# Optimization experiments

Measured on AMD Instinct MI355X. Metric: run time of the kernel, lower is better.

The kernel has to match this reference:

```python
import jax, jax.numpy as jnp
import numpy as np

WIDTH = 4096
NUM_HEADS = 8
BLOCK_W = WIDTH // NUM_HEADS


def _block_diag_linear(x, w, b):
    # x: [n, width] -> [n, h, bw]; w: [h, bw, bw]; b: [h, bw]
    n = x.shape[0]
    xh = x.reshape(n, NUM_HEADS, BLOCK_W)
    y = jnp.einsum('nhi,hij->nhj', xh, w) + b
    return y.reshape(n, WIDTH)


def setup_inputs() -> dict:
    key = jax.random.key(0)
    ks = jax.random.split(key, 7)
    n = 8192
    x = jax.random.normal(ks[0], (n, WIDTH), dtype=jnp.float32)
    s = jnp.sort(jax.random.randint(ks[1], (n,), 0, 8, dtype=jnp.int32))
    # a_param init: uniform on ring radii [0.9, 0.999], softplus-inverse transform
    eps = 1e-8
    u = jax.random.uniform(ks[2], (WIDTH,), minval=0.9**2 + eps, maxval=0.999**2 + eps)
    t = 0.5 * jnp.log(u)
    a_param = jnp.log(jnp.exp(-t) - 1.0).astype(jnp.float32)
    std = 1.0 / np.sqrt(BLOCK_W)
    ig_w = std * jax.random.normal(ks[3], (NUM_HEADS, BLOCK_W, BLOCK_W), dtype=jnp.float32)
    ig_b = jnp.zeros((NUM_HEADS, BLOCK_W), dtype=jnp.float32)
    ag_w = std * jax.random.normal(ks[4], (NUM_HEADS, BLOCK_W, BLOCK_W), dtype=jnp.float32)
    ag_b = jnp.zeros((NUM_HEADS, BLOCK_W), dtype=jnp.float32)
    return {'x': x, 's': s, 'a_param': a_param, 'ig_w': ig_w, 'ig_b': ig_b,
            'ag_w': ag_w, 'ag_b': ag_b}


def reference(x, s, a_param, ig_w, ig_b, ag_w, ag_b):
    n, k = x.shape
    # reset mask: True at position 0 and wherever segment id changes
    reset = jnp.concatenate([jnp.ones((1,), dtype=bool), s[1:] != s[:-1]])
    gate_x = jax.nn.sigmoid(_block_diag_linear(x, ig_w, ig_b))
    gate_a = jax.nn.sigmoid(_block_diag_linear(x, ag_w, ag_b))
    log_a = -8.0 * gate_a * jax.nn.softplus(a_param)  # [n, k]
    a = jnp.exp(log_a)
    a_square = jnp.exp(2.0 * log_a)
    multiplier = jnp.sqrt(1.0 - a_square)
    multiplier = jnp.where(reset[:, None], 1.0, multiplier)
    normalized_x = x * gate_x * multiplier
    # linear recurrence h[t] = a[t] * h[t-1] + normalized_x[t] via parallel scan
    def combine(e1, e2):
        a1, b1 = e1
        a2, b2 = e2
        return (a1 * a2, a2 * b1 + b2)
    _, out = jax.lax.associative_scan(combine, (a, normalized_x), axis=0)
    return out
```

## Files before the change

kernel.cpp:

```cpp
#include <hip/hip_runtime.h>
#include <hip/hip_bf16.h>
#include <stdint.h>

#define WIDTH 4096
#define NROWS 8192
#define NHEADS 8
#define BW 512
#define CS 128
#define NCHUNK (NROWS/CS)

typedef short bf16x8 __attribute__((ext_vector_type(8)));
typedef float f32x4 __attribute__((ext_vector_type(4)));

__device__ __forceinline__ uint32_t rne_bf16(float f) {
  uint32_t u = __float_as_uint(f);
  return (u + 0x7fffu + ((u >> 16) & 1u)) >> 16;
}
__device__ __forceinline__ uint32_t pack2(float lo, float hi) {
  return rne_bf16(lo) | (rne_bf16(hi) << 16);
}
__device__ __forceinline__ float bf16_to_f32(uint32_t bits) {
  return __uint_as_float(bits << 16);
}

__device__ __forceinline__ void gload_lds16(const void* g, void* l) {
  __builtin_amdgcn_global_load_lds(
      (const __attribute__((address_space(1))) void*)g,
      (__attribute__((address_space(3))) void*)l, 16, 0, 0);
}

__global__ void prep_xbf16(const float* __restrict__ x, uint16_t* __restrict__ xb) {
  size_t i = ((size_t)blockIdx.x * 256 + threadIdx.x) * 8;
  float4 f0 = *reinterpret_cast<const float4*>(x + i);
  float4 f1 = *reinterpret_cast<const float4*>(x + i + 4);
  uint4 v;
  v.x = pack2(f0.x, f0.y); v.y = pack2(f0.z, f0.w);
  v.z = pack2(f1.x, f1.y); v.w = pack2(f1.z, f1.w);
  *reinterpret_cast<uint4*>(xb + i) = v;
}

__global__ void prep_weights(const float* __restrict__ ig_w,
                             const float* __restrict__ ag_w,
                             uint16_t* __restrict__ wt) {
  __shared__ float tile[32][33];
  int j0 = blockIdx.x * 32;
  int i0 = blockIdx.y * 32;
  int m  = blockIdx.z;
  const float* src = ((m >> 3) ? ag_w : ig_w) + (size_t)(m & 7) * BW * BW;
  int tx = threadIdx.x & 31, ty = threadIdx.x >> 5;
  #pragma unroll
  for (int k = 0; k < 4; k++) {
    int i = i0 + ty + 8 * k;
    tile[ty + 8 * k][tx] = src[(size_t)i * BW + (j0 + tx)];
  }
  __syncthreads();
  #pragma unroll
  for (int k = 0; k < 4; k++) {
    int j = j0 + ty + 8 * k;
    wt[((size_t)m * BW + j) * BW + (i0 + tx)] = (uint16_t)rne_bf16(tile[tx][ty + 8 * k]);
  }
}

__global__ void prep_misc(const float* __restrict__ a_param, float* __restrict__ cvec) {
  int i = blockIdx.x * 256 + threadIdx.x;
  if (i < WIDTH) {
    float x = a_param[i];
    float sp = (x > 15.f) ? x : log1pf(expf(x));
    cvec[i] = 8.f * sp;
  }
}

#define BM 128
#define BN 64
#define BK 64

__global__ __launch_bounds__(256, 4)
void gates_gemm(const uint16_t* __restrict__ xb,
                const int* __restrict__ s,
                const uint16_t* __restrict__ wt,
                const float* __restrict__ ig_b,
                const float* __restrict__ ag_b,
                const float* __restrict__ cvec,
                uint32_t* __restrict__ lanx,
                float* __restrict__ cA,
                float* __restrict__ cB) {
  __shared__ __align__(16) unsigned char dsm[32768];
  __shared__ unsigned char resetm[BM];

  const int b = blockIdx.x;
  const int orig = (b & 7) * 512 + (b >> 3);
  const int h  = orig >> 9;
  const int rem = orig & 511;
  const int mt = rem >> 3;
  const int nt = rem & 7;
  const int m0 = mt * BM;
  const int j0 = nt * BN;

  const int tid = threadIdx.x;
  const int lane = tid & 63;
  const int w = tid >> 6;
  const int wr = w >> 1;
  const int wc = w & 1;
  const int lrow = lane & 15;
  const int lkg  = lane >> 4;

  if (tid < BM) {
    int n = m0 + tid;
    resetm[tid] = (n == 0) || (s[n] != s[n - 1]);
  }

  const char* xb_src[4];
  #pragma unroll
  for (int i = 0; i < 4; i++) {
    int o = i * 4096 + tid * 16;
    int row = o >> 7;
    int c = (o & 127) ^ ((row & 7) << 4);
    xb_src[i] = (const char*)xb + (size_t)(m0 + row) * (WIDTH * 2) + h * (BW * 2) + c;
  }
  const char* w_src[4];
  #pragma unroll
  for (int i = 0; i < 4; i++) {
    int o = i * 4096 + tid * 16;
    int g = o >> 13;
    int jl = (o >> 7) & 63;
    int c = (o & 127) ^ ((jl & 7) << 4);
    w_src[i] = (const char*)wt + ((size_t)((g * 8 + h) * BW + (j0 + jl))) * (BW * 2) + c;
  }

  f32x4 acc[2][4][2];
  #pragma unroll
  for (int g = 0; g < 2; g++)
    #pragma unroll
    for (int mf = 0; mf < 4; mf++)
      #pragma unroll
      for (int nf = 0; nf < 2; nf++)
        acc[g][mf][nf] = (f32x4){0.f, 0.f, 0.f, 0.f};

  for (int kt = 0; kt < 8; kt++) {
    const int p = (nt + 1 + kt) & 7;
    __syncthreads();
    #pragma unroll
    for (int i = 0; i < 4; i++)
      gload_lds16(xb_src[i] + p * 128, dsm + i * 4096 + tid * 16);
    #pragma unroll
    for (int i = 0; i < 4; i++)
      gload_lds16(w_src[i] + p * 128, dsm + 16384 + i * 4096 + tid * 16);
    __syncthreads();
    #pragma unroll
    for (int ks = 0; ks < 2; ks++) {
      bf16x8 af[4];
      #pragma unroll
      for (int mf = 0; mf < 4; mf++) {
        int row = wr * 64 + 16 * mf + lrow;
        uint32_t addr = (uint32_t)((row << 7) + ks * 64 + lkg * 16);
        addr ^= (uint32_t)((row & 7) << 4);
        af[mf] = *reinterpret_cast<const bf16x8*>(dsm + addr);
      }
      #pragma unroll
      for (int g = 0; g < 2; g++) {
        #pragma unroll
        for (int nf = 0; nf < 2; nf++) {
          int j = wc * 32 + 16 * nf + lrow;
          uint32_t addr = (uint32_t)(16384 + (g << 13) + (j << 7) + ks * 64 + lkg * 16);
          addr ^= (uint32_t)((j & 7) << 4);
          bf16x8 bfr = *reinterpret_cast<const bf16x8*>(dsm + addr);
          #pragma unroll
          for (int mf = 0; mf < 4; mf++) {
            acc[g][mf][nf] = __builtin_amdgcn_mfma_f32_16x16x32_bf16(
                af[mf], bfr, acc[g][mf][nf], 0, 0, 0);
          }
        }
      }
    }
  }
  __syncthreads();

  float* smf = (float*)(dsm + 16384);

  #pragma unroll
  for (int nf = 0; nf < 2; nf++) {
    int jl = wc * 32 + 16 * nf + lrow;
    int jj = h * BW + j0 + jl;
    const int cc2 = jl * 2;
    float igb = ig_b[jj], agb = ag_b[jj], cv = cvec[jj];
    float segA[4], segB[4];
    #pragma unroll
    for (int mf = 0; mf < 4; mf++) {
      float A = 1.f, B = 0.f;
      int rbase = wr * 64 + 16 * mf + 4 * lkg;
      #pragma unroll
      for (int r = 0; r < 4; r++) {
        int row = rbase + r;
        int n = m0 + row;
        size_t o = (size_t)n * WIDTH + jj;
        float yig = acc[0][mf][nf][r] + igb;
        float yag = acc[1][mf][nf][r] + agb;
        float gx = __builtin_amdgcn_rcpf(1.f + __expf(-yig));
        float ga = __builtin_amdgcn_rcpf(1.f + __expf(-yag));
        float la = -ga * cv;
        uint32_t la_bits = rne_bf16(la);
        float la_r = bf16_to_f32(la_bits);
        float a = __expf(la_r);
        float mult = resetm[row] ? 1.f
                     : __builtin_amdgcn_sqrtf(fmaxf(1.f - a * a, 0.f));
        uint32_t xaddr = (uint32_t)((row << 7) + cc2) ^ (uint32_t)((row & 7) << 4);
        float xv = bf16_to_f32(*reinterpret_cast<const uint16_t*>(dsm + xaddr));
        float nx = xv * gx * mult;
        uint32_t nx_bits = rne_bf16(nx);
        float nx_r = bf16_to_f32(nx_bits);
        lanx[o] = la_bits | (nx_bits << 16);
        A *= a;
        B = fmaf(a, B, nx_r);
      }
      segA[mf] = A; segB[mf] = B;
    }
    #pragma unroll
    for (int mf = 0; mf < 4; mf++) {
      float A = segA[mf], B = segB[mf];
      #pragma unroll
      for (int d = 16; d <= 32; d <<= 1) {
        float pA = __shfl_xor(A, d, 64);
        float pB = __shfl_xor(B, d, 64);
        bool up = (lane & d) != 0;
        B = up ? fmaf(A, pB, B) : fmaf(pA, B, pB);
        A *= pA;
      }
      segA[mf] = A; segB[mf] = B;
    }
    float colA = segA[0], colB = segB[0];
    #pragma unroll
    for (int mf = 1; mf < 4; mf++) {
      colB = fmaf(segA[mf], colB, segB[mf]);
      colA *= segA[mf];
    }
    if (lkg == 0) {
      int clocal = wc * 32 + 16 * nf + lrow;
      smf[wr * 64 + clocal] = colA;
      smf[128 + wr * 64 + clocal] = colB;
    }
  }
  __syncthreads();
  if (tid < BN) {
    float A0 = smf[tid],       B0 = smf[128 + tid];
    float A1 = smf[64 + tid],  B1 = smf[192 + tid];
    float Af = A0 * A1;
    float Bf = fmaf(A1, B0, B1);
    int jj = h * BW + j0 + tid;
    cA[mt * WIDTH + jj] = Af;
    cB[mt * WIDTH + jj] = Bf;
  }
}

__global__ void scan_prefix(const float* __restrict__ cA, const float* __restrict__ cB,
                            float* __restrict__ prefix) {
  int c = blockIdx.x * 256 + threadIdx.x;
  float hcur = 0.f;
  for (int i0 = 0; i0 < NCHUNK; i0 += 8) {
    float av[8], bv[8];
    #pragma unroll
    for (int e = 0; e < 8; e++) { av[e] = cA[(i0 + e) * WIDTH + c]; bv[e] = cB[(i0 + e) * WIDTH + c]; }
    #pragma unroll
    for (int e = 0; e < 8; e++) { prefix[(i0 + e) * WIDTH + c] = hcur; hcur = av[e] * hcur + bv[e]; }
  }
}

__global__ void scan_apply(const uint32_t* __restrict__ lanx,
                           const float* __restrict__ prefix,
                           float* __restrict__ out) {
  int chunk = blockIdx.x;
  int c0 = (blockIdx.y * 256 + threadIdx.x) * 4;
  size_t base = (size_t)chunk * CS * WIDTH + c0;
  float h[4];
  #pragma unroll
  for (int q = 0; q < 4; q++) h[q] = prefix[chunk * WIDTH + c0 + q];
  for (int rb = 0; rb < CS; rb += 4) {
    uint4 v[4];
    #pragma unroll
    for (int e = 0; e < 4; e++)
      v[e] = *reinterpret_cast<const uint4*>(lanx + base + (size_t)(rb + e) * WIDTH);
    #pragma unroll
    for (int e = 0; e < 4; e++) {
      float4 ov;
      h[0] = fmaf(__expf(bf16_to_f32(v[e].x & 0xffffu)), h[0], bf16_to_f32(v[e].x >> 16)); ov.x = h[0];
      h[1] = fmaf(__expf(bf16_to_f32(v[e].y & 0xffffu)), h[1], bf16_to_f32(v[e].y >> 16)); ov.y = h[1];
      h[2] = fmaf(__expf(bf16_to_f32(v[e].z & 0xffffu)), h[2], bf16_to_f32(v[e].z >> 16)); ov.z = h[2];
      h[3] = fmaf(__expf(bf16_to_f32(v[e].w & 0xffffu)), h[3], bf16_to_f32(v[e].w >> 16)); ov.w = h[3];
      *reinterpret_cast<float4*>(out + base + (size_t)(rb + e) * WIDTH) = ov;
    }
  }
}

extern "C" void kernel_launch(void* const* d_in, const int* in_sizes, int n_in,
                              void* d_out, int out_size, void* d_ws, size_t ws_size,
                              hipStream_t stream) {
  const float* x       = (const float*)d_in[0];
  const int*   s       = (const int*)d_in[1];
  const float* a_param = (const float*)d_in[2];
  const float* ig_w    = (const float*)d_in[3];
  const float* ig_b    = (const float*)d_in[4];
  const float* ag_w    = (const float*)d_in[5];
  const float* ag_b    = (const float*)d_in[6];
  float* out = (float*)d_out;
  char* ws = (char*)d_ws;

  uint32_t* lanx   = (uint32_t*)ws;
  uint16_t* wt     = (uint16_t*)(ws + 134217728);
  uint16_t* xb     = (uint16_t*)(ws + 142606336);
  float*    cvec   = (float*)(ws + 209715200);
  float*    cA     = (float*)(ws + 209731584);
  float*    cB     = (float*)(ws + 210780160);
  float*    prefix = (float*)(ws + 211828736);

  prep_xbf16<<<dim3(16384), 256, 0, stream>>>(x, xb);
  prep_weights<<<dim3(16, 16, 16), 256, 0, stream>>>(ig_w, ag_w, wt);
  prep_misc<<<dim3(16), 256, 0, stream>>>(a_param, cvec);
  gates_gemm<<<dim3(4096), 256, 0, stream>>>(xb, s, wt, ig_b, ag_b, cvec,
                                             lanx, cA, cB);
  scan_prefix<<<dim3(16), 256, 0, stream>>>(cA, cB, prefix);
  scan_apply<<<dim3(NCHUNK, 4), 256, 0, stream>>>(lanx, prefix, out);
}
```

Measured before the change: 224.7 us.

## Fuse x bf16 conversion into GEMM by loading fp32 x tiles into LDS

Removes the separate prep kernel that converted x to bf16. The GEMM now streams fp32 x tiles straight into a larger LDS buffer and converts them to bf16 in registers with v_cvt_pk_bf16_f32 before the MFMA. This drops a full read and write pass over x, but each GEMM block now reads twice as many x bytes. The larger LDS footprint also lowers the occupancy target from 4 to 3 blocks. The epilogue loop is reordered to handle both column fragments per row, and the epilogue now uses fp32 x values rather than bf16-rounded ones.

```diff
diff --git a/kernel.cpp b/kernel.cpp
--- a/kernel.cpp
+++ b/kernel.cpp
@@ -22,21 +22,16 @@
 __device__ __forceinline__ float bf16_to_f32(uint32_t bits) {
   return __uint_as_float(bits << 16);
 }
+__device__ __forceinline__ uint32_t cvtpk(float a, float b) {
+  uint32_t r;
+  asm("v_cvt_pk_bf16_f32 %0, %1, %2" : "=v"(r) : "v"(a), "v"(b));
+  return r;
+}
 
 __device__ __forceinline__ void gload_lds16(const void* g, void* l) {
   __builtin_amdgcn_global_load_lds(
       (const __attribute__((address_space(1))) void*)g,
       (__attribute__((address_space(3))) void*)l, 16, 0, 0);
-}
-
-__global__ void prep_xbf16(const float* __restrict__ x, uint16_t* __restrict__ xb) {
-  size_t i = ((size_t)blockIdx.x * 256 + threadIdx.x) * 8;
-  float4 f0 = *reinterpret_cast<const float4*>(x + i);
-  float4 f1 = *reinterpret_cast<const float4*>(x + i + 4);
-  uint4 v;
-  v.x = pack2(f0.x, f0.y); v.y = pack2(f0.z, f0.w);
-  v.z = pack2(f1.x, f1.y); v.w = pack2(f1.z, f1.w);
-  *reinterpret_cast<uint4*>(xb + i) = v;
 }
 
 __global__ void prep_weights(const float* __restrict__ ig_w,
@@ -74,8 +69,8 @@
 #define BN 64
 #define BK 64
 
-__global__ __launch_bounds__(256, 4)
-void gates_gemm(const uint16_t* __restrict__ xb,
+__global__ __launch_bounds__(256, 3)
+void gates_gemm(const float* __restrict__ x,
                 const int* __restrict__ s,
                 const uint16_t* __restrict__ wt,
                 const float* __restrict__ ig_b,
@@ -84,7 +79,7 @@
                 uint32_t* __restrict__ lanx,
                 float* __restrict__ cA,
                 float* __restrict__ cB) {
-  __shared__ __align__(16) unsigned char dsm[32768];
+  __shared__ __align__(16) unsigned char dsm[49152];
   __shared__ unsigned char resetm[BM];
 
   const int b = blockIdx.x;
@@ -109,13 +104,13 @@
     resetm[tid] = (n == 0) || (s[n] != s[n - 1]);
   }
 
-  const char* xb_src[4];
-  #pragma unroll
-  for (int i = 0; i < 4; i++) {
+  const char* x_src[8];
+  #pragma unroll
+  for (int i = 0; i < 8; i++) {
     int o = i * 4096 + tid * 16;
-    int row = o >> 7;
-    int c = (o & 127) ^ ((row & 7) << 4);
-    xb_src[i] = (const char*)xb + (size_t)(m0 + row) * (WIDTH * 2) + h * (BW * 2) + c;
+    int row = o >> 8;
+    int c = (o & 255) ^ ((row & 7) << 5);
+    x_src[i] = (const char*)x + ((size_t)(m0 + row) * WIDTH + h * BW) * 4 + c;
   }
   const char* w_src[4];
   #pragma unroll
@@ -140,11 +135,11 @@
     const int p = (nt + 1 + kt) & 7;
     __syncthreads();
     #pragma unroll
+    for (int i = 0; i < 8; i++)
+      gload_lds16(x_src[i] + p * 256, dsm + i * 4096 + tid * 16);
+    #pragma unroll
     for (int i = 0; i < 4; i++)
-      gload_lds16(xb_src[i] + p * 128, dsm + i * 4096 + tid * 16);
-    #pragma unroll
-    for (int i = 0; i < 4; i++)
-      gload_lds16(w_src[i] + p * 128, dsm + 16384 + i * 4096 + tid * 16);
+      gload_lds16(w_src[i] + p * 128, dsm + 32768 + i * 4096 + tid * 16);
     __syncthreads();
     #pragma unroll
     for (int ks = 0; ks < 2; ks++) {
@@ -152,16 +147,23 @@
       #pragma unroll
       for (int mf = 0; mf < 4; mf++) {
         int row = wr * 64 + 16 * mf + lrow;
-        uint32_t addr = (uint32_t)((row << 7) + ks * 64 + lkg * 16);
-        addr ^= (uint32_t)((row & 7) << 4);
-        af[mf] = *reinterpret_cast<const bf16x8*>(dsm + addr);
+        uint32_t addr = (uint32_t)((row << 8) + ks * 128 + lkg * 32);
+        addr ^= (uint32_t)((row & 7) << 5);
+        f32x4 lo = *reinterpret_cast<const f32x4*>(dsm + addr);
+        f32x4 hi = *reinterpret_cast<const f32x4*>(dsm + addr + 16);
+        union { uint32_t u[4]; bf16x8 v; } cvu;
+        cvu.u[0] = cvtpk(lo.x, lo.y);
+        cvu.u[1] = cvtpk(lo.z, lo.w);
+        cvu.u[2] = cvtpk(hi.x, hi.y);
+        cvu.u[3] = cvtpk(hi.z, hi.w);
+        af[mf] = cvu.v;
       }
       #pragma unroll
       for (int g = 0; g < 2; g++) {
         #pragma unroll
         for (int nf = 0; nf < 2; nf++) {
           int j = wc * 32 + 16 * nf + lrow;
-          uint32_t addr = (uint32_t)(16384 + (g << 13) + (j << 7) + ks * 64 + lkg * 16);
+          uint32_t addr = (uint32_t)(32768 + (g << 13) + (j << 7) + ks * 64 + lkg * 16);
           addr ^= (uint32_t)((j & 7) << 4);
           bf16x8 bfr = *reinterpret_cast<const bf16x8*>(dsm + addr);
           #pragma unroll
@@ -175,48 +177,58 @@
   }
   __syncthreads();
 
-  float* smf = (float*)(dsm + 16384);
-
+  float* smf = (float*)(dsm + 32768);
+
+  const int jl0 = wc * 32 + lrow;
+  float igb[2], agb[2], cv2[2];
   #pragma unroll
   for (int nf = 0; nf < 2; nf++) {
-    int jl = wc * 32 + 16 * nf + lrow;
-    int jj = h * BW + j0 + jl;
-    const int cc2 = jl * 2;
-    float igb = ig_b[jj], agb = ag_b[jj], cv = cvec[jj];
-    float segA[4], segB[4];
-    #pragma unroll
-    for (int mf = 0; mf < 4; mf++) {
-      float A = 1.f, B = 0.f;
-      int rbase = wr * 64 + 16 * mf + 4 * lkg;
-      #pragma unroll
-      for (int r = 0; r < 4; r++) {
-        int row = rbase + r;
-        int n = m0 + row;
-        size_t o = (size_t)n * WIDTH + jj;
-        float yig = acc[0][mf][nf][r] + igb;
-        float yag = acc[1][mf][nf][r] + agb;
+    int jj = h * BW + j0 + jl0 + 16 * nf;
+    igb[nf] = ig_b[jj]; agb[nf] = ag_b[jj]; cv2[nf] = cvec[jj];
+  }
+
+  float segA[2][4], segB[2][4];
+  #pragma unroll
+  for (int mf = 0; mf < 4; mf++) {
+    float A[2] = {1.f, 1.f}, B[2] = {0.f, 0.f};
+    int rbase = wr * 64 + 16 * mf + 4 * lkg;
+    #pragma unroll
+    for (int r = 0; r < 4; r++) {
+      int row = rbase + r;
+      int n = m0 + row;
+      bool rs = resetm[row] != 0;
+      #pragma unroll
+      for (int nf = 0; nf < 2; nf++) {
+        int jl = jl0 + 16 * nf;
+        size_t o = (size_t)n * WIDTH + h * BW + j0 + jl;
+        float yig = acc[0][mf][nf][r] + igb[nf];
+        float yag = acc[1][mf][nf][r] + agb[nf];
         float gx = __builtin_amdgcn_rcpf(1.f + __expf(-yig));
         float ga = __builtin_amdgcn_rcpf(1.f + __expf(-yag));
-        float la = -ga * cv;
+        float la = -ga * cv2[nf];
         uint32_t la_bits = rne_bf16(la);
         float la_r = bf16_to_f32(la_bits);
         float a = __expf(la_r);
-        float mult = resetm[row] ? 1.f
+        float mult = rs ? 1.f
                      : __builtin_amdgcn_sqrtf(fmaxf(1.f - a * a, 0.f));
-        uint32_t xaddr = (uint32_t)((row << 7) + cc2) ^ (uint32_t)((row & 7) << 4);
-        float xv = bf16_to_f32(*reinterpret_cast<const uint16_t*>(dsm + xaddr));
+        uint32_t xaddr = (uint32_t)((row << 8) + jl * 4) ^ (uint32_t)((row & 7) << 5);
+        float xv = *reinterpret_cast<const float*>(dsm + xaddr);
         float nx = xv * gx * mult;
         uint32_t nx_bits = rne_bf16(nx);
         float nx_r = bf16_to_f32(nx_bits);
         lanx[o] = la_bits | (nx_bits << 16);
-        A *= a;
-        B = fmaf(a, B, nx_r);
+        A[nf] *= a;
+        B[nf] = fmaf(a, B[nf], nx_r);
       }
-      segA[mf] = A; segB[mf] = B;
-    }
+    }
+    segA[0][mf] = A[0]; segB[0][mf] = B[0];
+    segA[1][mf] = A[1]; segB[1][mf] = B[1];
+  }
+  #pragma unroll
+  for (int nf = 0; nf < 2; nf++) {
     #pragma unroll
     for (int mf = 0; mf < 4; mf++) {
-      float A = segA[mf], B = segB[mf];
+      float A = segA[nf][mf], B = segB[nf][mf];
       #pragma unroll
       for (int d = 16; d <= 32; d <<= 1) {
         float pA = __shfl_xor(A, d, 64);
@@ -225,13 +237,13 @@
         B = up ? fmaf(A, pB, B) : fmaf(pA, B, pB);
         A *= pA;
       }
-      segA[mf] = A; segB[mf] = B;
-    }
-    float colA = segA[0], colB = segB[0];
+      segA[nf][mf] = A; segB[nf][mf] = B;
+    }
+    float colA = segA[nf][0], colB = segB[nf][0];
     #pragma unroll
     for (int mf = 1; mf < 4; mf++) {
-      colB = fmaf(segA[mf], colB, segB[mf]);
-      colA *= segA[mf];
+      colB = fmaf(segA[nf][mf], colB, segB[nf][mf]);
+      colA *= segA[nf][mf];
     }
     if (lkg == 0) {
       int clocal = wc * 32 + 16 * nf + lrow;
@@ -305,16 +317,14 @@
 
   uint32_t* lanx   = (uint32_t*)ws;
   uint16_t* wt     = (uint16_t*)(ws + 134217728);
-  uint16_t* xb     = (uint16_t*)(ws + 142606336);
-  float*    cvec   = (float*)(ws + 209715200);
-  float*    cA     = (float*)(ws + 209731584);
-  float*    cB     = (float*)(ws + 210780160);
-  float*    prefix = (float*)(ws + 211828736);
-
-  prep_xbf16<<<dim3(16384), 256, 0, stream>>>(x, xb);
+  float*    cvec   = (float*)(ws + 142606336);
+  float*    cA     = (float*)(ws + 142622720);
+  float*    cB     = (float*)(ws + 143671296);
+  float*    prefix = (float*)(ws + 144719872);
+
   prep_weights<<<dim3(16, 16, 16), 256, 0, stream>>>(ig_w, ag_w, wt);
   prep_misc<<<dim3(16), 256, 0, stream>>>(a_param, cvec);
-  gates_gemm<<<dim3(4096), 256, 0, stream>>>(xb, s, wt, ig_b, ag_b, cvec,
+  gates_gemm<<<dim3(4096), 256, 0, stream>>>(x, s, wt, ig_b, ag_b, cvec,
                                              lanx, cA, cB);
   scan_prefix<<<dim3(16), 256, 0, stream>>>(cA, cB, prefix);
   scan_apply<<<dim3(NCHUNK, 4), 256, 0, stream>>>(lanx, prefix, out);
```

After: 199.6 us. -11.2%, faster.

## Fuse chunk scan into gates GEMM with decoupled look-back across chunks

Applied to the files above, without the earlier changes.

The separate scan_prefix and scan_apply kernels are replaced by a single-pass decoupled look-back scan inside the gates GEMM. Blocks take an atomic ticket so chunks are processed in order, publish their chunk aggregates and inclusive prefixes through flags, and write the final output directly from registers. This removes the 128MB packed intermediate write and re-read plus two kernel launches. In exchange it adds register pressure (launch bounds lowered to 3), inter-block spin-waiting, and a small zeroing kernel.

```diff
diff --git a/kernel.cpp b/kernel.cpp
--- a/kernel.cpp
+++ b/kernel.cpp
@@ -7,7 +7,9 @@
 #define NHEADS 8
 #define BW 512
 #define CS 128
-#define NCHUNK (NROWS/CS)
+#define NCHUNK 64
+#define NGROUP 64
+#define NSLOT 65
 
 typedef short bf16x8 __attribute__((ext_vector_type(8)));
 typedef float f32x4 __attribute__((ext_vector_type(4)));
@@ -70,33 +72,51 @@
   }
 }
 
+__global__ void zero_sync(uint32_t* __restrict__ flags, float* __restrict__ Hbuf,
+                          uint32_t* __restrict__ ticket) {
+  int i = blockIdx.x * 256 + threadIdx.x;
+  if (i < NGROUP * NSLOT) flags[i] = ((i % NSLOT) == 0) ? 2u : 0u;
+  if (i < NGROUP * 64) {
+    int g = i >> 6, t = i & 63;
+    Hbuf[(size_t)(g * NSLOT) * 64 + t] = 0.f;
+  }
+  if (i == 0) *ticket = 0u;
+}
+
 #define BM 128
 #define BN 64
 #define BK 64
 
-__global__ __launch_bounds__(256, 4)
+__global__ __launch_bounds__(256, 3)
 void gates_gemm(const uint16_t* __restrict__ xb,
                 const int* __restrict__ s,
                 const uint16_t* __restrict__ wt,
                 const float* __restrict__ ig_b,
                 const float* __restrict__ ag_b,
                 const float* __restrict__ cvec,
-                uint32_t* __restrict__ lanx,
-                float* __restrict__ cA,
-                float* __restrict__ cB) {
+                float* __restrict__ out,
+                float* __restrict__ aggA,
+                float* __restrict__ aggB,
+                float* __restrict__ Hbuf,
+                uint32_t* __restrict__ flags,
+                uint32_t* __restrict__ ticket) {
   __shared__ __align__(16) unsigned char dsm[32768];
   __shared__ unsigned char resetm[BM];
-
-  const int b = blockIdx.x;
-  const int orig = (b & 7) * 512 + (b >> 3);
-  const int h  = orig >> 9;
-  const int rem = orig & 511;
-  const int mt = rem >> 3;
-  const int nt = rem & 7;
-  const int m0 = mt * BM;
+  __shared__ int tkshare;
+  __shared__ int kshare;
+
+  const int tid = threadIdx.x;
+  if (tid == 0) tkshare = (int)atomicAdd(ticket, 1u);
+  __syncthreads();
+  const int tk = tkshare;
+  const int c  = tk >> 6;
+  const int g  = tk & 63;
+  const int h  = g >> 3;
+  const int nt = g & 7;
+  const int m0 = c * BM;
   const int j0 = nt * BN;
-
-  const int tid = threadIdx.x;
+  const int sc = c + 1;
+
   const int lane = tid & 63;
   const int w = tid >> 6;
   const int wr = w >> 1;
@@ -114,27 +134,27 @@
   for (int i = 0; i < 4; i++) {
     int o = i * 4096 + tid * 16;
     int row = o >> 7;
-    int c = (o & 127) ^ ((row & 7) << 4);
-    xb_src[i] = (const char*)xb + (size_t)(m0 + row) * (WIDTH * 2) + h * (BW * 2) + c;
+    int cc = (o & 127) ^ ((row & 7) << 4);
+    xb_src[i] = (const char*)xb + (size_t)(m0 + row) * (WIDTH * 2) + h * (BW * 2) + cc;
   }
   const char* w_src[4];
   #pragma unroll
   for (int i = 0; i < 4; i++) {
     int o = i * 4096 + tid * 16;
-    int g = o >> 13;
+    int gg = o >> 13;
     int jl = (o >> 7) & 63;
-    int c = (o & 127) ^ ((jl & 7) << 4);
-    w_src[i] = (const char*)wt + ((size_t)((g * 8 + h) * BW + (j0 + jl))) * (BW * 2) + c;
+    int cc = (o & 127) ^ ((jl & 7) << 4);
+    w_src[i] = (const char*)wt + ((size_t)((gg * 8 + h) * BW + (j0 + jl))) * (BW * 2) + cc;
   }
 
   f32x4 acc[2][4][2];
   #pragma unroll
-  for (int g = 0; g < 2; g++)
+  for (int gg = 0; gg < 2; gg++)
     #pragma unroll
     for (int mf = 0; mf < 4; mf++)
       #pragma unroll
       for (int nf = 0; nf < 2; nf++)
-        acc[g][mf][nf] = (f32x4){0.f, 0.f, 0.f, 0.f};
+        acc[gg][mf][nf] = (f32x4){0.f, 0.f, 0.f, 0.f};
 
   for (int kt = 0; kt < 8; kt++) {
     const int p = (nt + 1 + kt) & 7;
@@ -157,17 +177,17 @@
         af[mf] = *reinterpret_cast<const bf16x8*>(dsm + addr);
       }
       #pragma unroll
-      for (int g = 0; g < 2; g++) {
+      for (int gg = 0; gg < 2; gg++) {
         #pragma unroll
         for (int nf = 0; nf < 2; nf++) {
           int j = wc * 32 + 16 * nf + lrow;
-          uint32_t addr = (uint32_t)(16384 + (g << 13) + (j << 7) + ks * 64 + lkg * 16);
+          uint32_t addr = (uint32_t)(16384 + (gg << 13) + (j << 7) + ks * 64 + lkg * 16);
           addr ^= (uint32_t)((j & 7) << 4);
           bf16x8 bfr = *reinterpret_cast<const bf16x8*>(dsm + addr);
           #pragma unroll
           for (int mf = 0; mf < 4; mf++) {
-            acc[g][mf][nf] = __builtin_amdgcn_mfma_f32_16x16x32_bf16(
-                af[mf], bfr, acc[g][mf][nf], 0, 0, 0);
+            acc[gg][mf][nf] = __builtin_amdgcn_mfma_f32_16x16x32_bf16(
+                af[mf], bfr, acc[gg][mf][nf], 0, 0, 0);
           }
         }
       }
@@ -177,13 +197,20 @@
 
   float* smf = (float*)(dsm + 16384);
 
+  const int jl0 = wc * 32 + lrow;
+  float igb[2], agb[2], cv2[2];
   #pragma unroll
   for (int nf = 0; nf < 2; nf++) {
-    int jl = wc * 32 + 16 * nf + lrow;
-    int jj = h * BW + j0 + jl;
-    const int cc2 = jl * 2;
-    float igb = ig_b[jj], agb = ag_b[jj], cv = cvec[jj];
-    float segA[4], segB[4];
+    int jj = h * BW + j0 + jl0 + 16 * nf;
+    igb[nf] = ig_b[jj]; agb[nf] = ag_b[jj]; cv2[nf] = cvec[jj];
+  }
+
+  float a_r[4][2][4], nx_r[4][2][4];
+  float preA[4][2], preB[4][2];
+
+  #pragma unroll
+  for (int nf = 0; nf < 2; nf++) {
+    float mA = 1.f, mB = 0.f;
     #pragma unroll
     for (int mf = 0; mf < 4; mf++) {
       float A = 1.f, B = 0.f;
@@ -191,101 +218,128 @@
       #pragma unroll
       for (int r = 0; r < 4; r++) {
         int row = rbase + r;
-        int n = m0 + row;
-        size_t o = (size_t)n * WIDTH + jj;
-        float yig = acc[0][mf][nf][r] + igb;
-        float yag = acc[1][mf][nf][r] + agb;
+        float yig = acc[0][mf][nf][r] + igb[nf];
+        float yag = acc[1][mf][nf][r] + agb[nf];
         float gx = __builtin_amdgcn_rcpf(1.f + __expf(-yig));
         float ga = __builtin_amdgcn_rcpf(1.f + __expf(-yag));
-        float la = -ga * cv;
-        uint32_t la_bits = rne_bf16(la);
-        float la_r = bf16_to_f32(la_bits);
+        float la = -ga * cv2[nf];
+        float la_r = bf16_to_f32(rne_bf16(la));
         float a = __expf(la_r);
-        float mult = resetm[row] ? 1.f
+        float mult = (resetm[row] != 0) ? 1.f
                      : __builtin_amdgcn_sqrtf(fmaxf(1.f - a * a, 0.f));
-        uint32_t xaddr = (uint32_t)((row << 7) + cc2) ^ (uint32_t)((row & 7) << 4);
+        int jl = jl0 + 16 * nf;
+        uint32_t xaddr = (uint32_t)((row << 7) + jl * 2) ^ (uint32_t)((row & 7) << 4);
         float xv = bf16_to_f32(*reinterpret_cast<const uint16_t*>(dsm + xaddr));
         float nx = xv * gx * mult;
-        uint32_t nx_bits = rne_bf16(nx);
-        float nx_r = bf16_to_f32(nx_bits);
-        lanx[o] = la_bits | (nx_bits << 16);
+        float nxr = bf16_to_f32(rne_bf16(nx));
+        a_r[mf][nf][r] = a;
+        nx_r[mf][nf][r] = nxr;
         A *= a;
-        B = fmaf(a, B, nx_r);
-      }
-      segA[mf] = A; segB[mf] = B;
-    }
-    #pragma unroll
-    for (int mf = 0; mf < 4; mf++) {
-      float A = segA[mf], B = segB[mf];
-      #pragma unroll
-      for (int d = 16; d <= 32; d <<= 1) {
-        float pA = __shfl_xor(A, d, 64);
-        float pB = __shfl_xor(B, d, 64);
-        bool up = (lane & d) != 0;
-        B = up ? fmaf(A, pB, B) : fmaf(pA, B, pB);
-        A *= pA;
-      }
-      segA[mf] = A; segB[mf] = B;
-    }
-    float colA = segA[0], colB = segB[0];
-    #pragma unroll
-    for (int mf = 1; mf < 4; mf++) {
-      colB = fmaf(segA[mf], colB, segB[mf]);
-      colA *= segA[mf];
+        B = fmaf(a, B, nxr);
+      }
+      float Ai = A, Bi = B;
+      float pA = __shfl_up(Ai, 16, 64);
+      float pB = __shfl_up(Bi, 16, 64);
+      if (lkg >= 1) { Bi = fmaf(Ai, pB, Bi); Ai *= pA; }
+      pA = __shfl_up(Ai, 32, 64);
+      pB = __shfl_up(Bi, 32, 64);
+      if (lkg >= 2) { Bi = fmaf(Ai, pB, Bi); Ai *= pA; }
+      float eA = __shfl_up(Ai, 16, 64);
+      float eB = __shfl_up(Bi, 16, 64);
+      if (lkg == 0) { eA = 1.f; eB = 0.f; }
+      int src = (lane & 15) + 48;
+      float tA = __shfl(Ai, src, 64);
+      float tB = __shfl(Bi, src, 64);
+      preA[mf][nf] = mA * eA;
+      preB[mf][nf] = fmaf(eA, mB, eB);
+      mB = fmaf(tA, mB, tB);
+      mA *= tA;
     }
     if (lkg == 0) {
-      int clocal = wc * 32 + 16 * nf + lrow;
-      smf[wr * 64 + clocal] = colA;
-      smf[128 + wr * 64 + clocal] = colB;
-    }
-  }
-  __syncthreads();
-  if (tid < BN) {
-    float A0 = smf[tid],       B0 = smf[128 + tid];
-    float A1 = smf[64 + tid],  B1 = smf[192 + tid];
-    float Af = A0 * A1;
-    float Bf = fmaf(A1, B0, B1);
-    int jj = h * BW + j0 + tid;
-    cA[mt * WIDTH + jj] = Af;
-    cB[mt * WIDTH + jj] = Bf;
-  }
-}
-
-__global__ void scan_prefix(const float* __restrict__ cA, const float* __restrict__ cB,
-                            float* __restrict__ prefix) {
-  int c = blockIdx.x * 256 + threadIdx.x;
-  float hcur = 0.f;
-  for (int i0 = 0; i0 < NCHUNK; i0 += 8) {
-    float av[8], bv[8];
-    #pragma unroll
-    for (int e = 0; e < 8; e++) { av[e] = cA[(i0 + e) * WIDTH + c]; bv[e] = cB[(i0 + e) * WIDTH + c]; }
-    #pragma unroll
-    for (int e = 0; e < 8; e++) { prefix[(i0 + e) * WIDTH + c] = hcur; hcur = av[e] * hcur + bv[e]; }
-  }
-}
-
-__global__ void scan_apply(const uint32_t* __restrict__ lanx,
-                           const float* __restrict__ prefix,
-                           float* __restrict__ out) {
-  int chunk = blockIdx.x;
-  int c0 = (blockIdx.y * 256 + threadIdx.x) * 4;
-  size_t base = (size_t)chunk * CS * WIDTH + c0;
-  float h[4];
-  #pragma unroll
-  for (int q = 0; q < 4; q++) h[q] = prefix[chunk * WIDTH + c0 + q];
-  for (int rb = 0; rb < CS; rb += 4) {
-    uint4 v[4];
-    #pragma unroll
-    for (int e = 0; e < 4; e++)
-      v[e] = *reinterpret_cast<const uint4*>(lanx + base + (size_t)(rb + e) * WIDTH);
-    #pragma unroll
-    for (int e = 0; e < 4; e++) {
-      float4 ov;
-      h[0] = fmaf(__expf(bf16_to_f32(v[e].x & 0xffffu)), h[0], bf16_to_f32(v[e].x >> 16)); ov.x = h[0];
-      h[1] = fmaf(__expf(bf16_to_f32(v[e].y & 0xffffu)), h[1], bf16_to_f32(v[e].y >> 16)); ov.y = h[1];
-      h[2] = fmaf(__expf(bf16_to_f32(v[e].z & 0xffffu)), h[2], bf16_to_f32(v[e].z >> 16)); ov.z = h[2];
-      h[3] = fmaf(__expf(bf16_to_f32(v[e].w & 0xffffu)), h[3], bf16_to_f32(v[e].w >> 16)); ov.w = h[3];
-      *reinterpret_cast<float4*>(out + base + (size_t)(rb + e) * WIDTH) = ov;
+      int cl = wc * 32 + 16 * nf + lrow;
+      smf[wr * 64 + cl] = mA;
+      smf[128 + wr * 64 + cl] = mB;
+    }
+  }
+  __syncthreads();
+
+  const size_t eslot = (size_t)g * NSLOT + sc;
+  float cAv = 0.f, cBv = 0.f;
+  if (tid < 64) {
+    float A0 = smf[tid],      B0 = smf[128 + tid];
+    float A1 = smf[64 + tid], B1 = smf[192 + tid];
+    cAv = A0 * A1;
+    cBv = fmaf(A1, B0, B1);
+    __hip_atomic_store(&aggA[eslot * 64 + tid], cAv, __ATOMIC_RELAXED, __HIP_MEMORY_SCOPE_AGENT);
+    __hip_atomic_store(&aggB[eslot * 64 + tid], cBv, __ATOMIC_RELAXED, __HIP_MEMORY_SCOPE_AGENT);
+  }
+  __syncthreads();
+  if (tid == 0)
+    __hip_atomic_store(&flags[eslot], 1u, __ATOMIC_RELEASE, __HIP_MEMORY_SCOPE_AGENT);
+
+  if (tid == 0) {
+    int k = sc - 1;
+    while (true) {
+      uint32_t f = __hip_atomic_load(&flags[g * NSLOT + k], __ATOMIC_ACQUIRE,
+                                     __HIP_MEMORY_SCOPE_AGENT);
+      if (f == 2u) break;
+      if (f == 1u) { k--; continue; }
+      __builtin_amdgcn_s_sleep(2);
+    }
+    kshare = k;
+  }
+  __syncthreads();
+  {
+    int k = kshare;
+    if (tid < 64) {
+      float P = __hip_atomic_load(&Hbuf[((size_t)g * NSLOT + k) * 64 + tid],
+                                  __ATOMIC_RELAXED, __HIP_MEMORY_SCOPE_AGENT);
+      for (int i = k + 1; i < sc; ++i) {
+        float Ai = __hip_atomic_load(&aggA[((size_t)g * NSLOT + i) * 64 + tid],
+                                     __ATOMIC_RELAXED, __HIP_MEMORY_SCOPE_AGENT);
+        float Bi = __hip_atomic_load(&aggB[((size_t)g * NSLOT + i) * 64 + tid],
+                                     __ATOMIC_RELAXED, __HIP_MEMORY_SCOPE_AGENT);
+        P = fmaf(Ai, P, Bi);
+      }
+      smf[256 + tid] = P;
+      float Hc = fmaf(cAv, P, cBv);
+      __hip_atomic_store(&Hbuf[eslot * 64 + tid], Hc, __ATOMIC_RELAXED,
+                         __HIP_MEMORY_SCOPE_AGENT);
+    }
+  }
+  __syncthreads();
+  if (tid == 0)
+    __hip_atomic_store(&flags[eslot], 2u, __ATOMIC_RELEASE, __HIP_MEMORY_SCOPE_AGENT);
+
+  float h0[2];
+  #pragma unroll
+  for (int nf = 0; nf < 2; nf++) {
+    int cl = wc * 32 + 16 * nf + lrow;
+    float P = smf[256 + cl];
+    if (wr == 1) {
+      float A0 = smf[cl], B0 = smf[128 + cl];
+      h0[nf] = fmaf(A0, P, B0);
+    } else {
+      h0[nf] = P;
+    }
+  }
+  #pragma unroll
+  for (int mf = 0; mf < 4; mf++) {
+    float hseg[2];
+    #pragma unroll
+    for (int nf = 0; nf < 2; nf++)
+      hseg[nf] = fmaf(preA[mf][nf], h0[nf], preB[mf][nf]);
+    int rbase = wr * 64 + 16 * mf + 4 * lkg;
+    #pragma unroll
+    for (int r = 0; r < 4; r++) {
+      int n = m0 + rbase + r;
+      size_t ob = (size_t)n * WIDTH + h * BW + j0;
+      #pragma unroll
+      for (int nf = 0; nf < 2; nf++) {
+        int cl = wc * 32 + 16 * nf + lrow;
+        hseg[nf] = fmaf(a_r[mf][nf][r], hseg[nf], nx_r[mf][nf][r]);
+        out[ob + cl] = hseg[nf];
+      }
     }
   }
 }
@@ -303,19 +357,19 @@
   float* out = (float*)d_out;
   char* ws = (char*)d_ws;
 
-  uint32_t* lanx   = (uint32_t*)ws;
-  uint16_t* wt     = (uint16_t*)(ws + 134217728);
-  uint16_t* xb     = (uint16_t*)(ws + 142606336);
-  float*    cvec   = (float*)(ws + 209715200);
-  float*    cA     = (float*)(ws + 209731584);
-  float*    cB     = (float*)(ws + 210780160);
-  float*    prefix = (float*)(ws + 211828736);
+  uint16_t* wt     = (uint16_t*)ws;
+  uint16_t* xb     = (uint16_t*)(ws + 8388608);
+  float*    cvec   = (float*)(ws + 75497472);
+  float*    aggA   = (float*)(ws + 75513856);
+  float*    aggB   = (float*)(ws + 76578816);
+  float*    Hbuf   = (float*)(ws + 77643776);
+  uint32_t* flags  = (uint32_t*)(ws + 78708736);
+  uint32_t* ticket = (uint32_t*)(ws + 78725376);
 
   prep_xbf16<<<dim3(16384), 256, 0, stream>>>(x, xb);
   prep_weights<<<dim3(16, 16, 16), 256, 0, stream>>>(ig_w, ag_w, wt);
   prep_misc<<<dim3(16), 256, 0, stream>>>(a_param, cvec);
+  zero_sync<<<dim3(17), 256, 0, stream>>>(flags, Hbuf, ticket);
   gates_gemm<<<dim3(4096), 256, 0, stream>>>(xb, s, wt, ig_b, ag_b, cvec,
-                                             lanx, cA, cB);
-  scan_prefix<<<dim3(16), 256, 0, stream>>>(cA, cB, prefix);
-  scan_apply<<<dim3(NCHUNK, 4), 256, 0, stream>>>(lanx, prefix, out);
-}
+                                             out, aggA, aggB, Hbuf, flags, ticket);
+}
```

After: 545.6 us. 2.43x slower.
